# Kernel tuning notes

Measured on AMD Instinct MI355X. Metric: run time of the kernel, lower is better.

Reference implementation:

```python
import jax, jax.numpy as jnp
import numpy as np

B, T, C = 2, 2048, 2048
N_HEAD, N_KV_HEAD = 16, 4
HEAD_DIM = C // N_HEAD          # 128
N_REP = N_HEAD // N_KV_HEAD    # 4
WINDOW = 512


def setup_inputs() -> dict:
    key = jax.random.key(0)
    k1, k2, k3 = jax.random.split(key, 3)
    x = jax.random.normal(k1, (B, T, C), dtype=jnp.float32)
    w_attn = jax.random.normal(k2, (C, (N_HEAD + 2 * N_KV_HEAD) * HEAD_DIM), dtype=jnp.float32) * 0.02
    w_proj = jax.random.normal(k3, (C, C), dtype=jnp.float32) * 0.02
    # RoPE cos/sin table: [T, HEAD_DIM//2, 2]
    inv_freq = 1.0 / (10000.0 ** (jnp.arange(0, HEAD_DIM, 2, dtype=jnp.float32) / HEAD_DIM))
    ang = jnp.arange(T, dtype=jnp.float32)[:, None] * inv_freq[None, :]
    freqs_cis = jnp.stack([jnp.cos(ang), jnp.sin(ang)], axis=-1)
    mask = jnp.ones((T, T), dtype=bool)  # True = masked (except window, forced allowed)
    return {"x": x, "w_attn": w_attn, "w_proj": w_proj, "freqs_cis": freqs_cis, "mask": mask}


def _apply_rope(t, freqs_cis):
    # t: [B, T, H, D]; freqs_cis: [T, D//2, 2] (cos, sin)
    b, s, h, d = t.shape
    tp = t.reshape(b, s, h, d // 2, 2)
    cos = freqs_cis[:, None, :, 0]  # [T,1,D/2]
    sin = freqs_cis[:, None, :, 1]
    tr = tp[..., 0] * cos - tp[..., 1] * sin
    ti = tp[..., 0] * sin + tp[..., 1] * cos
    return jnp.stack([tr, ti], axis=-1).reshape(b, s, h, d)


def reference(x, w_attn, w_proj, freqs_cis, mask):
    qkv = x @ w_attn  # [B,T,(H+2KV)*D]
    q_size = N_HEAD * HEAD_DIM
    kv_size = N_KV_HEAD * HEAD_DIM
    q = qkv[..., :q_size].reshape(B, T, N_HEAD, HEAD_DIM)
    k = qkv[..., q_size:q_size + kv_size].reshape(B, T, N_KV_HEAD, HEAD_DIM)
    v = qkv[..., q_size + kv_size:].reshape(B, T, N_KV_HEAD, HEAD_DIM)
    q = _apply_rope(q, freqs_cis)
    k = _apply_rope(k, freqs_cis)
    # GQA repeat_kv
    k = jnp.repeat(k, N_REP, axis=2)
    v = jnp.repeat(v, N_REP, axis=2)
    q = q.transpose(0, 2, 1, 3)  # [B,H,T,D]
    k = k.transpose(0, 2, 1, 3)
    v = v.transpose(0, 2, 1, 3)
    # effective mask: window positions forced allowed, rest per input mask
    i = jnp.arange(T)[:, None]
    j = jnp.arange(T)[None, :]
    in_window = (j <= i) & (i - j < WINDOW)
    effective = mask & ~in_window  # True = masked (-inf)
    scores = jnp.einsum("bhqd,bhkd->bhqk", q, k) / jnp.sqrt(jnp.float32(HEAD_DIM))
    scores = jnp.where(effective[None, None], -jnp.inf, scores)
    attn = jax.nn.softmax(scores, axis=-1)
    y = jnp.einsum("bhqk,bhkd->bhqd", attn, v)
    y = y.transpose(0, 2, 1, 3).reshape(B, T, C)
    return y @ w_proj
```

## Files before the change

### kernel.cpp

```cpp
#include <hip/hip_runtime.h>
#include <hip/hip_bf16.h>

typedef __attribute__((ext_vector_type(8))) short short8;
typedef __attribute__((ext_vector_type(4))) float f32x4;

#define MFMA16(a,b,c) __builtin_amdgcn_mfma_f32_16x16x32_bf16((a),(b),(c),0,0,0)

static __device__ __forceinline__ unsigned short f2b(float f){
  __hip_bfloat16 h = __float2bfloat16(f);
  return __builtin_bit_cast(unsigned short, h);
}
static __device__ __forceinline__ float b2f(unsigned short u){
  unsigned int v = ((unsigned int)u)<<16;
  return __builtin_bit_cast(float, v);
}

static __device__ __forceinline__ void gld_lds16(const void* g, void* l){
  __builtin_amdgcn_global_load_lds((const __attribute__((address_space(1))) unsigned int*)g,
                                   (__attribute__((address_space(3))) unsigned int*)l, 16, 0, 0);
}

__global__ __launch_bounds__(256) void k_prep(const float* __restrict__ x,
    const float* __restrict__ wA, const float* __restrict__ wP,
    unsigned short* __restrict__ xb, unsigned short* __restrict__ wtA,
    unsigned short* __restrict__ wtP){
  int bid = blockIdx.x, tid = threadIdx.x;
  if (bid < 4096){
    int i = (bid*256 + tid)*8;
    float4 a = *(const float4*)(x+i);
    float4 b = *(const float4*)(x+i+4);
    short8 v;
    v[0]=f2b(a.x); v[1]=f2b(a.y); v[2]=f2b(a.z); v[3]=f2b(a.w);
    v[4]=f2b(b.x); v[5]=f2b(b.y); v[6]=f2b(b.z); v[7]=f2b(b.w);
    *(short8*)(xb+i) = v;
    return;
  }
  __shared__ float tile[32][33];
  const float* in; unsigned short* out; int R, C, bx, by;
  if (bid < 10240){ int tt = bid-4096;  in=wA; out=wtA; R=2048; C=3072; bx=tt%96; by=tt/96; }
  else            { int tt = bid-10240; in=wP; out=wtP; R=2048; C=2048; bx=tt%64; by=tt/64; }
  int c0 = bx*32, r0 = by*32;
  int tx = tid&31, ty = tid>>5;
  #pragma unroll
  for (int i=0;i<4;i++) tile[ty*4+i][tx] = in[(size_t)(r0+ty*4+i)*C + c0+tx];
  __syncthreads();
  #pragma unroll
  for (int i=0;i<4;i++) out[(size_t)(c0+ty*4+i)*R + r0+tx] = f2b(tile[tx][ty*4+i]);
}

template<int OB>
__global__ __launch_bounds__(256,2) void k_gemm97(const unsigned short* __restrict__ A,
    const unsigned short* __restrict__ BT, void* __restrict__ Cv,
    int M, int N, int K, int nbx){
  __shared__ __align__(16) unsigned short As[128*64];
  __shared__ __align__(16) unsigned short Bs[128*64];
  const int NT = K >> 6;
  int cpx = gridDim.x >> 3;
  int bid = blockIdx.x;
  int swz = (bid & 7)*cpx + (bid >> 3);
  int bm = (swz / nbx)*128, bn = (swz % nbx)*128;
  int tid = threadIdx.x;
  int wave = tid >> 6, lane = tid & 63;
  int r = lane & 15, g = lane >> 4;
  int wr = (wave >> 1)*64, wc = (wave & 1)*64;
  int sw = r & 7;

  f32x4 acc[4][4];
  #pragma unroll
  for (int i=0;i<4;i++)
    #pragma unroll
    for (int j=0;j<4;j++){ acc[i][j][0]=0.f; acc[i][j][1]=0.f; acc[i][j][2]=0.f; acc[i][j][3]=0.f; }

  for (int t=0; t<NT; ++t){
    #pragma unroll
    for (int i=0;i<4;i++){
      int c = i*256 + tid;
      int row = c>>3, kc = c&7;
      gld_lds16(&A[(size_t)(bm+row)*K + (size_t)t*64 + ((kc^(row&7))*8)], (char*)As + c*16);
    }
    #pragma unroll
    for (int i=0;i<4;i++){
      int c = i*256 + tid;
      int row = c>>3, kc = c&7;
      gld_lds16(&BT[(size_t)(bn+row)*K + (size_t)t*64 + ((kc^(row&7))*8)], (char*)Bs + c*16);
    }
    __syncthreads();
    short8 af[4][2], bf[4][2];
    #pragma unroll
    for (int i=0;i<4;i++)
      #pragma unroll
      for (int kk=0;kk<2;kk++){
        int row = wr + i*16 + r;
        af[i][kk] = *(const short8*)((const char*)As + ((size_t)(row*8 + ((kk*4+g)^sw))<<4));
      }
    #pragma unroll
    for (int j=0;j<4;j++)
      #pragma unroll
      for (int kk=0;kk<2;kk++){
        int row = wc + j*16 + r;
        bf[j][kk] = *(const short8*)((const char*)Bs + ((size_t)(row*8 + ((kk*4+g)^sw))<<4));
      }
    #pragma unroll
    for (int kk=0;kk<2;kk++)
      #pragma unroll
      for (int i=0;i<4;i++)
        #pragma unroll
        for (int j=0;j<4;j++)
          acc[i][j] = MFMA16(af[i][kk], bf[j][kk], acc[i][j]);
    __syncthreads();
  }

  #pragma unroll
  for (int i=0;i<4;i++)
    #pragma unroll
    for (int j=0;j<4;j++)
      #pragma unroll
      for (int rr=0;rr<4;rr++){
        size_t idx = (size_t)(bm + wr + i*16 + 4*g + rr)*N + bn + wc + j*16 + r;
        if (OB) ((unsigned short*)Cv)[idx] = f2b(acc[i][j][rr]);
        else    ((float*)Cv)[idx] = acc[i][j][rr];
      }
}

__global__ __launch_bounds__(256) void k_rope_split(const unsigned short* __restrict__ qkv,
    const float* __restrict__ fc, unsigned short* __restrict__ qb,
    unsigned short* __restrict__ kb, unsigned short* __restrict__ vb){
  int row = blockIdx.x;
  int t = row & 2047, b = row >> 11;
  int tid = threadIdx.x;
  const unsigned short* qr = qkv + (size_t)row*3072;
  const float QS = 0.12751743f;
  #pragma unroll
  for (int ii=0; ii<4; ii++){
    int p = tid + 256*ii;
    int h = p>>6, f = p&63;
    unsigned int pr = *(const unsigned int*)&qr[h*128 + 2*f];
    float x0 = b2f((unsigned short)(pr & 0xffff)), x1 = b2f((unsigned short)(pr >> 16));
    float2 cssn = *(const float2*)&fc[t*128 + 2*f];
    float o0 = (x0*cssn.x - x1*cssn.y)*QS, o1 = (x0*cssn.y + x1*cssn.x)*QS;
    size_t o = ((size_t)(b*16 + h)*2048 + t)*128 + 2*f;
    qb[o] = f2b(o0); qb[o+1] = f2b(o1);
  }
  {
    int p = tid; int kh = p>>6, f = p&63;
    unsigned int pr = *(const unsigned int*)&qr[2048 + kh*128 + 2*f];
    float x0 = b2f((unsigned short)(pr & 0xffff)), x1 = b2f((unsigned short)(pr >> 16));
    float2 cssn = *(const float2*)&fc[t*128 + 2*f];
    float o0 = x0*cssn.x - x1*cssn.y, o1 = x0*cssn.y + x1*cssn.x;
    size_t o = ((size_t)(b*4 + kh)*2048 + t)*128 + 2*f;
    kb[o] = f2b(o0); kb[o+1] = f2b(o1);
  }
  #pragma unroll
  for (int ii=0; ii<2; ii++){
    int e = tid + 256*ii;
    int kh = e>>7, d = e&127;
    size_t o = ((size_t)(b*4 + kh)*2048 + t)*128 + d;
    vb[o] = qr[2560 + e];
  }
}

__global__ void k_transpose_v(const unsigned short* __restrict__ v,
                              unsigned short* __restrict__ vt){
  __shared__ unsigned short tile[32][33];
  int bk = blockIdx.z;
  int d0 = blockIdx.x*32, t0 = blockIdx.y*32;
  int tx = threadIdx.x, ty = threadIdx.y;
  const unsigned short* vp = v + (size_t)bk*2048*128;
  unsigned short* vtp = vt + (size_t)bk*128*2048;
  #pragma unroll
  for (int i=0;i<4;i++) tile[ty*4+i][tx] = vp[(t0+ty*4+i)*128 + d0+tx];
  __syncthreads();
  #pragma unroll
  for (int i=0;i<4;i++) vtp[(d0+ty*4+i)*2048 + t0+tx] = tile[tx][ty*4+i];
}

__global__ __launch_bounds__(256,2) void k_attn(const unsigned short* __restrict__ q,
    const unsigned short* __restrict__ k, const unsigned short* __restrict__ vt,
    unsigned short* __restrict__ y){
  int qb0 = blockIdx.x*64;
  int h = blockIdx.y, b = blockIdx.z;
  int kvh = h>>2;
  int tid = threadIdx.x, wave = tid>>6, lane = tid&63;
  int w0 = qb0 + wave*16;
  int r = lane&15, g = lane>>4;
  const unsigned short* qh = q + ((size_t)(b*16+h)*2048)*128;
  const unsigned short* kh = k + ((size_t)(b*4+kvh)*2048)*128;
  const unsigned short* vh = vt + ((size_t)(b*4+kvh)*128)*2048;

  __shared__ unsigned short Ks[2][64*128];
  __shared__ unsigned short Vs[2][128*64];
  __shared__ unsigned short plds[4][16][72];

  short8 qf[4];
  #pragma unroll
  for (int c=0;c<4;c++) qf[c] = *(const short8*)&qh[(w0+r)*128 + c*32 + g*8];

  f32x4 acc[8];
  #pragma unroll
  for (int d=0; d<8; d++){ acc[d][0]=0.f; acc[d][1]=0.f; acc[d][2]=0.f; acc[d][3]=0.f; }
  float m[4]  = {-1e30f,-1e30f,-1e30f,-1e30f};
  float ls[4] = {0.f,0.f,0.f,0.f};

  int lo = qb0 - 511; if (lo < 0) lo = 0;
  int t0 = lo & ~63;
  int nt = ((qb0 + 63) - t0)/64 + 1;
  int sw = (r&7)<<4;

  #define STAGE(bb, kt)                                                          \
    { _Pragma("unroll")                                                          \
      for (int p=0;p<4;p++){                                                     \
        int c = p*256 + tid;                                                     \
        int row = c>>4, col = (c&15)*16;                                         \
        gld_lds16((const char*)kh + (size_t)((kt)+row)*256 + (col ^ ((row&7)<<4)),\
                  (char*)&Ks[bb][0] + c*16);                                     \
      }                                                                          \
      _Pragma("unroll")                                                          \
      for (int p=0;p<4;p++){                                                     \
        int c = p*256 + tid;                                                     \
        int row = c>>3, col = (c&7)*16;                                          \
        gld_lds16((const char*)vh + (size_t)row*4096 + (size_t)(kt)*2 + (col ^ ((row&7)<<4)),\
                  (char*)&Vs[bb][0] + c*16);                                     \
      }                                                                          \
    }

  STAGE(0, t0);
  __syncthreads();
  int cur = 0;

  for (int it=0; it<nt; it++){
    int kt = t0 + it*64;
    if (it+1 < nt) STAGE(cur^1, t0 + (it+1)*64);

    bool use = (kt <= w0+15) && (kt+63 >= w0-511);
    if (use){
      f32x4 S[4];
      #pragma unroll
      for (int s=0;s<4;s++){
        f32x4 a; a[0]=0.f; a[1]=0.f; a[2]=0.f; a[3]=0.f;
        const char* kr = (const char*)&Ks[cur][0] + (s*16+r)*256;
        #pragma unroll
        for (int c=0;c<4;c++){
          short8 kf = *(const short8*)(kr + ((c*64 + g*16) ^ sw));
          a = MFMA16(qf[c], kf, a);
        }
        S[s] = a;
      }
      #pragma unroll
      for (int rr=0;rr<4;rr++){
        int i = w0 + 4*g + rr;
        float mx = -3e38f;
        #pragma unroll
        for (int s=0;s<4;s++){
          int j = kt + s*16 + r;
          bool valid = (j <= i) && (i - j < 512);
          float sv = valid ? S[s][rr] : -3e38f;
          S[s][rr] = sv;
          mx = fmaxf(mx, sv);
        }
        mx = fmaxf(mx, __shfl_xor(mx, 1));
        mx = fmaxf(mx, __shfl_xor(mx, 2));
        mx = fmaxf(mx, __shfl_xor(mx, 4));
        mx = fmaxf(mx, __shfl_xor(mx, 8));
        float mn = fmaxf(m[rr], mx);
        float al = exp2f(m[rr] - mn);
        m[rr] = mn;
        float ps = 0.f;
        #pragma unroll
        for (int s=0;s<4;s++){
          float p = exp2f(S[s][rr] - mn);
          S[s][rr] = p;
          ps += p;
        }
        ls[rr] = ls[rr]*al + ps;
        #pragma unroll
        for (int d=0;d<8;d++) acc[d][rr] *= al;
      }
      #pragma unroll
      for (int rr=0;rr<4;rr++)
        #pragma unroll
        for (int s=0;s<4;s++)
          plds[wave][4*g+rr][s*16+r] = f2b(S[s][rr]);
      short8 pf0 = *(const short8*)&plds[wave][r][g*8];
      short8 pf1 = *(const short8*)&plds[wave][r][32 + g*8];
      #pragma unroll
      for (int d=0;d<8;d++){
        const char* vr = (const char*)&Vs[cur][0] + (d*16+r)*128;
        short8 vf0 = *(const short8*)(vr + ((g*16) ^ sw));
        short8 vf1 = *(const short8*)(vr + ((64 + g*16) ^ sw));
        acc[d] = MFMA16(pf0, vf0, acc[d]);
        acc[d] = MFMA16(pf1, vf1, acc[d]);
      }
    }
    __syncthreads();
    cur ^= 1;
  }

  #pragma unroll
  for (int rr=0;rr<4;rr++){
    float s = ls[rr];
    s += __shfl_xor(s, 1);
    s += __shfl_xor(s, 2);
    s += __shfl_xor(s, 4);
    s += __shfl_xor(s, 8);
    float inv = 1.f/s;
    int i = w0 + 4*g + rr;
    #pragma unroll
    for (int d=0;d<8;d++)
      y[((size_t)(b*2048)+i)*2048 + h*128 + d*16 + r] = f2b(acc[d][rr]*inv);
  }
}

extern "C" void kernel_launch(void* const* d_in, const int* in_sizes, int n_in,
                              void* d_out, int out_size, void* d_ws, size_t ws_size,
                              hipStream_t stream) {
  const float* x      = (const float*)d_in[0];
  const float* w_attn = (const float*)d_in[1];
  const float* w_proj = (const float*)d_in[2];
  const float* fc     = (const float*)d_in[3];
  float* out = (float*)d_out;
  char* ws = (char*)d_ws;
  unsigned short* xb   = (unsigned short*)(ws);
  unsigned short* wtA  = (unsigned short*)(ws + 16777216);
  unsigned short* wtP  = (unsigned short*)(ws + 29360128);
  unsigned short* qkvb = (unsigned short*)(ws + 37748736);
  unsigned short* yb   = (unsigned short*)(ws + 37748736);
  unsigned short* qb   = (unsigned short*)(ws + 62914560);
  unsigned short* kb   = (unsigned short*)(ws + 79691776);
  unsigned short* vb   = (unsigned short*)(ws + 83886080);
  unsigned short* vtb  = (unsigned short*)(ws + 88080384);

  k_prep<<<14336, 256, 0, stream>>>(x, w_attn, w_proj, xb, wtA, wtP);
  k_gemm97<1><<<dim3(768), 256, 0, stream>>>(xb, wtA, qkvb, 4096, 3072, 2048, 24);
  k_rope_split<<<4096, 256, 0, stream>>>(qkvb, fc, qb, kb, vb);
  k_transpose_v<<<dim3(4,64,8), dim3(32,8), 0, stream>>>(vb, vtb);
  k_attn<<<dim3(32,16,2), 256, 0, stream>>>(qb, kb, vtb, yb);
  k_gemm97<0><<<dim3(512), 256, 0, stream>>>(yb, wtP, out, 4096, 2048, 2048, 16);
}
```

Before: 181.3 us.

## Process two 16-row query tiles per wave in sliding-window attention

Each attention block now covers 128 queries instead of 64, with every wave handling two 16-row query tiles (A and B) that share each staged K/V tile from LDS. This halves the grid and cuts the number of K/V tile loads per query, reusing each LDS fragment for twice the MFMA work. In exchange, register pressure roughly doubles (two accumulator sets), which may lower occupancy or cause spills. The grid also drops to 512 blocks, and tiles where only one of the two query groups is active still compute both.

```diff
diff --git a/kernel.cpp b/kernel.cpp
--- a/kernel.cpp
+++ b/kernel.cpp
@@ -177,11 +177,11 @@
 __global__ __launch_bounds__(256,2) void k_attn(const unsigned short* __restrict__ q,
     const unsigned short* __restrict__ k, const unsigned short* __restrict__ vt,
     unsigned short* __restrict__ y){
-  int qb0 = blockIdx.x*64;
+  int qb0 = blockIdx.x*128;
   int h = blockIdx.y, b = blockIdx.z;
   int kvh = h>>2;
   int tid = threadIdx.x, wave = tid>>6, lane = tid&63;
-  int w0 = qb0 + wave*16;
+  int w0A = qb0 + wave*32, w0B = w0A + 16;
   int r = lane&15, g = lane>>4;
   const unsigned short* qh = q + ((size_t)(b*16+h)*2048)*128;
   const unsigned short* kh = k + ((size_t)(b*4+kvh)*2048)*128;
@@ -191,19 +191,27 @@
   __shared__ unsigned short Vs[2][128*64];
   __shared__ unsigned short plds[4][16][72];
 
-  short8 qf[4];
-  #pragma unroll
-  for (int c=0;c<4;c++) qf[c] = *(const short8*)&qh[(w0+r)*128 + c*32 + g*8];
-
-  f32x4 acc[8];
-  #pragma unroll
-  for (int d=0; d<8; d++){ acc[d][0]=0.f; acc[d][1]=0.f; acc[d][2]=0.f; acc[d][3]=0.f; }
-  float m[4]  = {-1e30f,-1e30f,-1e30f,-1e30f};
-  float ls[4] = {0.f,0.f,0.f,0.f};
+  short8 qfA[4], qfB[4];
+  #pragma unroll
+  for (int c=0;c<4;c++){
+    qfA[c] = *(const short8*)&qh[(w0A+r)*128 + c*32 + g*8];
+    qfB[c] = *(const short8*)&qh[(w0B+r)*128 + c*32 + g*8];
+  }
+
+  f32x4 accA[8], accB[8];
+  #pragma unroll
+  for (int d=0; d<8; d++){
+    accA[d][0]=0.f; accA[d][1]=0.f; accA[d][2]=0.f; accA[d][3]=0.f;
+    accB[d][0]=0.f; accB[d][1]=0.f; accB[d][2]=0.f; accB[d][3]=0.f;
+  }
+  float mA[4]  = {-1e30f,-1e30f,-1e30f,-1e30f};
+  float mB[4]  = {-1e30f,-1e30f,-1e30f,-1e30f};
+  float lsA[4] = {0.f,0.f,0.f,0.f};
+  float lsB[4] = {0.f,0.f,0.f,0.f};
 
   int lo = qb0 - 511; if (lo < 0) lo = 0;
   int t0 = lo & ~63;
-  int nt = ((qb0 + 63) - t0)/64 + 1;
+  int nt = ((qb0 + 127) - t0)/64 + 1;
   int sw = (r&7)<<4;
 
   #define STAGE(bb, kt)                                                          \
@@ -229,66 +237,93 @@
 
   for (int it=0; it<nt; it++){
     int kt = t0 + it*64;
-    if (it+1 < nt) STAGE(cur^1, t0 + (it+1)*64);
-
-    bool use = (kt <= w0+15) && (kt+63 >= w0-511);
-    if (use){
-      f32x4 S[4];
+    if (it+1 < nt) STAGE(cur^1, kt + 64);
+
+    bool useA = (kt <= w0A+15) && (kt+63 >= w0A-511);
+    bool useB = (kt <= w0B+15) && (kt+63 >= w0B-511);
+    if (useA || useB){
+      f32x4 SA[4], SB[4];
       #pragma unroll
       for (int s=0;s<4;s++){
-        f32x4 a; a[0]=0.f; a[1]=0.f; a[2]=0.f; a[3]=0.f;
+        f32x4 aA; aA[0]=0.f; aA[1]=0.f; aA[2]=0.f; aA[3]=0.f;
+        f32x4 aB; aB[0]=0.f; aB[1]=0.f; aB[2]=0.f; aB[3]=0.f;
         const char* kr = (const char*)&Ks[cur][0] + (s*16+r)*256;
         #pragma unroll
         for (int c=0;c<4;c++){
           short8 kf = *(const short8*)(kr + ((c*64 + g*16) ^ sw));
-          a = MFMA16(qf[c], kf, a);
+          aA = MFMA16(qfA[c], kf, aA);
+          aB = MFMA16(qfB[c], kf, aB);
         }
-        S[s] = a;
-      }
+        SA[s] = aA; SB[s] = aB;
+      }
+      float mxA[4], mxB[4];
       #pragma unroll
       for (int rr=0;rr<4;rr++){
-        int i = w0 + 4*g + rr;
-        float mx = -3e38f;
+        int iA = w0A + 4*g + rr, iB = w0B + 4*g + rr;
+        float ma = -3e38f, mb_ = -3e38f;
         #pragma unroll
         for (int s=0;s<4;s++){
           int j = kt + s*16 + r;
-          bool valid = (j <= i) && (i - j < 512);
-          float sv = valid ? S[s][rr] : -3e38f;
-          S[s][rr] = sv;
-          mx = fmaxf(mx, sv);
+          bool vA = (j <= iA) && (iA - j < 512);
+          bool vB = (j <= iB) && (iB - j < 512);
+          float sa = vA ? SA[s][rr] : -3e38f;
+          float sb = vB ? SB[s][rr] : -3e38f;
+          SA[s][rr] = sa; SB[s][rr] = sb;
+          ma = fmaxf(ma, sa); mb_ = fmaxf(mb_, sb);
         }
-        mx = fmaxf(mx, __shfl_xor(mx, 1));
-        mx = fmaxf(mx, __shfl_xor(mx, 2));
-        mx = fmaxf(mx, __shfl_xor(mx, 4));
-        mx = fmaxf(mx, __shfl_xor(mx, 8));
-        float mn = fmaxf(m[rr], mx);
-        float al = exp2f(m[rr] - mn);
-        m[rr] = mn;
-        float ps = 0.f;
+        mxA[rr] = ma; mxB[rr] = mb_;
+      }
+      #pragma unroll
+      for (int st=1; st<16; st<<=1){
+        #pragma unroll
+        for (int rr=0;rr<4;rr++){
+          mxA[rr] = fmaxf(mxA[rr], __shfl_xor(mxA[rr], st));
+          mxB[rr] = fmaxf(mxB[rr], __shfl_xor(mxB[rr], st));
+        }
+      }
+      #pragma unroll
+      for (int rr=0;rr<4;rr++){
+        float mnA = fmaxf(mA[rr], mxA[rr]);
+        float mnB = fmaxf(mB[rr], mxB[rr]);
+        float alA = exp2f(mA[rr] - mnA);
+        float alB = exp2f(mB[rr] - mnB);
+        mA[rr] = mnA; mB[rr] = mnB;
+        float psA = 0.f, psB = 0.f;
         #pragma unroll
         for (int s=0;s<4;s++){
-          float p = exp2f(S[s][rr] - mn);
-          S[s][rr] = p;
-          ps += p;
+          float pa = exp2f(SA[s][rr] - mnA);
+          float pb = exp2f(SB[s][rr] - mnB);
+          SA[s][rr] = pa; SB[s][rr] = pb;
+          psA += pa; psB += pb;
         }
-        ls[rr] = ls[rr]*al + ps;
-        #pragma unroll
-        for (int d=0;d<8;d++) acc[d][rr] *= al;
+        lsA[rr] = lsA[rr]*alA + psA;
+        lsB[rr] = lsB[rr]*alB + psB;
+        #pragma unroll
+        for (int d=0;d<8;d++){ accA[d][rr] *= alA; accB[d][rr] *= alB; }
       }
       #pragma unroll
       for (int rr=0;rr<4;rr++)
         #pragma unroll
         for (int s=0;s<4;s++)
-          plds[wave][4*g+rr][s*16+r] = f2b(S[s][rr]);
-      short8 pf0 = *(const short8*)&plds[wave][r][g*8];
-      short8 pf1 = *(const short8*)&plds[wave][r][32 + g*8];
+          plds[wave][4*g+rr][s*16+r] = f2b(SA[s][rr]);
+      short8 pfA0 = *(const short8*)&plds[wave][r][g*8];
+      short8 pfA1 = *(const short8*)&plds[wave][r][32 + g*8];
+      #pragma unroll
+      for (int rr=0;rr<4;rr++)
+        #pragma unroll
+        for (int s=0;s<4;s++)
+          plds[wave][4*g+rr][s*16+r] = f2b(SB[s][rr]);
+      short8 pfB0 = *(const short8*)&plds[wave][r][g*8];
+      short8 pfB1 = *(const short8*)&plds[wave][r][32 + g*8];
       #pragma unroll
       for (int d=0;d<8;d++){
         const char* vr = (const char*)&Vs[cur][0] + (d*16+r)*128;
         short8 vf0 = *(const short8*)(vr + ((g*16) ^ sw));
         short8 vf1 = *(const short8*)(vr + ((64 + g*16) ^ sw));
-        acc[d] = MFMA16(pf0, vf0, acc[d]);
-        acc[d] = MFMA16(pf1, vf1, acc[d]);
+        accA[d] = MFMA16(pfA0, vf0, accA[d]);
+        accA[d] = MFMA16(pfA1, vf1, accA[d]);
+        accB[d] = MFMA16(pfB0, vf0, accB[d]);
+        accB[d] = MFMA16(pfB1, vf1, accB[d]);
       }
     }
     __syncthreads();
@@ -297,16 +332,16 @@
 
   #pragma unroll
   for (int rr=0;rr<4;rr++){
-    float s = ls[rr];
-    s += __shfl_xor(s, 1);
-    s += __shfl_xor(s, 2);
-    s += __shfl_xor(s, 4);
-    s += __shfl_xor(s, 8);
-    float inv = 1.f/s;
-    int i = w0 + 4*g + rr;
-    #pragma unroll
-    for (int d=0;d<8;d++)
-      y[((size_t)(b*2048)+i)*2048 + h*128 + d*16 + r] = f2b(acc[d][rr]*inv);
+    float sa = lsA[rr], sb = lsB[rr];
+    #pragma unroll
+    for (int st=1; st<16; st<<=1){ sa += __shfl_xor(sa, st); sb += __shfl_xor(sb, st); }
+    float invA = 1.f/sa, invB = 1.f/sb;
+    int iA = w0A + 4*g + rr, iB = w0B + 4*g + rr;
+    #pragma unroll
+    for (int d=0;d<8;d++){
+      y[((size_t)(b*2048)+iA)*2048 + h*128 + d*16 + r] = f2b(accA[d][rr]*invA);
+      y[((size_t)(b*2048)+iB)*2048 + h*128 + d*16 + r] = f2b(accB[d][rr]*invB);
+    }
   }
 }
 
@@ -333,6 +368,6 @@
   k_gemm97<1><<<dim3(768), 256, 0, stream>>>(xb, wtA, qkvb, 4096, 3072, 2048, 24);
   k_rope_split<<<4096, 256, 0, stream>>>(qkvb, fc, qb, kb, vb);
   k_transpose_v<<<dim3(4,64,8), dim3(32,8), 0, stream>>>(vb, vtb);
-  k_attn<<<dim3(32,16,2), 256, 0, stream>>>(qb, kb, vtb, yb);
+  k_attn<<<dim3(16,16,2), 256, 0, stream>>>(qb, kb, vtb, yb);
   k_gemm97<0><<<dim3(512), 256, 0, stream>>>(yb, wtP, out, 4096, 2048, 2048, 16);
 }
```

After: 175.0 us. -3.5%, faster.
